# Optimization experiments

Hardware: AMD Instinct MI355X
Metric: run time of the kernel (lower is better)

## Reference

```python
import jax, jax.numpy as jnp
import numpy as np

THRESH = 0.5   # spike_args['thresh']
LENS = 0.5     # spike_args['lens'] (surrogate gradient window)
DECAY = 0.2    # spike_args['decay']
XISHUSPIKE = 0.5
XISHUADA = 0.2

@jax.custom_vjp
def spike_fn(v):
    return (v > THRESH).astype(v.dtype)

def _spike_fwd(v):
    return spike_fn(v), v

def _spike_bwd(v, g):
    # rectangular surrogate: pass grad where |v - thresh| < lens
    return (g * (jnp.abs(v - THRESH) < LENS).astype(g.dtype),)

spike_fn.defvjp(_spike_fwd, _spike_bwd)

def setup_inputs() -> dict:
    key = jax.random.key(0)
    k1, k2, k3, k4 = jax.random.split(key, 4)
    B, IN, OUT = 512, 2048, 2048
    x = jax.random.normal(k1, (B, IN), jnp.float32)
    W_fc = jax.random.normal(k2, (OUT, IN), jnp.float32) / np.sqrt(IN).astype(np.float32)
    b_fc = jnp.zeros((OUT,), jnp.float32)
    W_rec = jax.random.normal(k3, (OUT, OUT), jnp.float32) / np.sqrt(OUT).astype(np.float32)
    b_rec = jnp.zeros((OUT,), jnp.float32)
    eye = jnp.eye(OUT, dtype=jnp.int32)
    keep = jax.random.bernoulli(k4, 0.5, (OUT, OUT)).astype(jnp.int32)
    rec_mask = (1 - eye) * keep
    return {"x": x, "W_fc": W_fc, "b_fc": b_fc, "W_rec": W_rec,
            "b_rec": b_rec, "rec_mask": rec_mask, "spike_window": 16}

def reference(x, W_fc, b_fc, W_rec, b_rec, rec_mask, spike_window):
    # feed-forward drive is constant across the time loop (same x each step, noise off)
    ff = x @ W_fc.T + b_fc                      # [B, OUT]
    Wr = W_rec * rec_mask.astype(W_rec.dtype)    # masked recurrent weight (idempotent)
    z = jnp.zeros_like(ff)

    def step(carry, _):
        mem, spk, ath, ssum = carry
        ath = 0.9 * ath + XISHUSPIKE * spk
        mem_ff = mem * DECAY * (1.0 - spk) + ff - ath * XISHUADA
        s_ff = spike_fn(mem_ff)
        mem_r = spk @ Wr.T + b_rec
        s_r = spike_fn(mem_r)
        mem = mem_ff + mem_r
        spk = s_ff + s_r
        ssum = ssum + spk
        return (mem, spk, ath, ssum), None

    (mem, spk, ath, ssum), _ = jax.lax.scan(step, (z, z, z, z), None, length=spike_window)
    return ssum
```

## Files before the change

### kernel.cpp

```cpp
#include <hip/hip_runtime.h>


#pragma clang fp contract(off)

#define B_ROWS 512
#define N_OUT 2048
#define K_IN 2048
#define NSTEP 16
#define NPANEL 4
#define PANK 512
#define BK 16
#define TM 64
#define TN 128
#define ASTR 68
#define BSTR 132
#define NTILES (PANK / BK)

__global__ __launch_bounds__(256) void transpose_tile(
    const float* __restrict__ W, const int* __restrict__ mask,
    float* __restrict__ WT, int useMask)
{
    __shared__ float t[32][33];
    int kb = blockIdx.x * 32, nb = blockIdx.y * 32;
    int tx = threadIdx.x, ty = threadIdx.y;
#pragma unroll
    for (int r = 0; r < 32; r += 8) {
        size_t src = (size_t)(nb + ty + r) * K_IN + (kb + tx);
        float v = W[src];
        if (useMask) v *= (float)mask[src];
        t[ty + r][tx] = v;
    }
    __syncthreads();
#pragma unroll
    for (int r = 0; r < 32; r += 8)
        WT[(size_t)(kb + ty + r) * N_OUT + (nb + tx)] = t[tx][ty + r];
}

__global__ __launch_bounds__(256) void init_state(float* mem, float* ath,
                                                  float* ssum, float* spk) {
    int idx = blockIdx.x * 256 + threadIdx.x;
    mem[idx] = 0.0f; ath[idx] = 0.0f; ssum[idx] = 0.0f; spk[idx] = 0.0f;
}

__global__ __launch_bounds__(128) void gemm_panel(
    const float* __restrict__ A,
    const float* __restrict__ BT,
    float* __restrict__ Cp)
{
    __shared__ float As[2][BK][ASTR];
    __shared__ float Bs[2][BK][BSTR];
    const int tid = threadIdx.x;
    const int tx = tid & 15;
    const int ty = tid >> 4;
    const int n0 = blockIdx.x * TN;
    const int m0 = blockIdx.y * TM;
    const int pan = blockIdx.z;
    const int kbase = pan * PANK;

    const int sa_m = tid >> 1;
    const int sa_k = (tid & 1) * 8;
    const int sb_k = tid >> 3;
    const int sb_n = (tid & 7) * 16;

    float acc[8][8];
#pragma unroll
    for (int i = 0; i < 8; i++)
#pragma unroll
        for (int j = 0; j < 8; j++) acc[i][j] = 0.0f;

    const float* Abase = A + (size_t)(m0 + sa_m) * K_IN + kbase + sa_k;
    const float* Bbase = BT + (size_t)(kbase + sb_k) * N_OUT + n0 + sb_n;

    float4 ra0, ra1, rb0, rb1, rb2, rb3;
    ra0 = *(const float4*)(Abase);
    ra1 = *(const float4*)(Abase + 4);
    rb0 = *(const float4*)(Bbase);
    rb1 = *(const float4*)(Bbase + 4);
    rb2 = *(const float4*)(Bbase + 8);
    rb3 = *(const float4*)(Bbase + 12);
    {
        float av[8] = {ra0.x, ra0.y, ra0.z, ra0.w, ra1.x, ra1.y, ra1.z, ra1.w};
#pragma unroll
        for (int j = 0; j < 8; j++) As[0][sa_k + j][sa_m] = av[j];
        *(float4*)&Bs[0][sb_k][sb_n]      = rb0;
        *(float4*)&Bs[0][sb_k][sb_n + 4]  = rb1;
        *(float4*)&Bs[0][sb_k][sb_n + 8]  = rb2;
        *(float4*)&Bs[0][sb_k][sb_n + 12] = rb3;
    }
    __syncthreads();

    int buf = 0;
    for (int kt = 0; kt < NTILES; kt++) {
        if (kt + 1 < NTILES) {
            const float* Ab = Abase + (kt + 1) * BK;
            const float* Bb = Bbase + (size_t)(kt + 1) * BK * N_OUT;
            ra0 = *(const float4*)(Ab);
            ra1 = *(const float4*)(Ab + 4);
            rb0 = *(const float4*)(Bb);
            rb1 = *(const float4*)(Bb + 4);
            rb2 = *(const float4*)(Bb + 8);
            rb3 = *(const float4*)(Bb + 12);
        }
#pragma unroll
        for (int kk = 0; kk < BK; kk++) {
            float4 a0 = *(const float4*)&As[buf][kk][ty * 8];
            float4 a1 = *(const float4*)&As[buf][kk][ty * 8 + 4];
            float4 b0 = *(const float4*)&Bs[buf][kk][tx * 8];
            float4 b1 = *(const float4*)&Bs[buf][kk][tx * 8 + 4];
            float aa[8] = {a0.x, a0.y, a0.z, a0.w, a1.x, a1.y, a1.z, a1.w};
            float bb[8] = {b0.x, b0.y, b0.z, b0.w, b1.x, b1.y, b1.z, b1.w};
#pragma unroll
            for (int i = 0; i < 8; i++)
#pragma unroll
                for (int j = 0; j < 8; j++)
                    acc[i][j] = fmaf(aa[i], bb[j], acc[i][j]);
        }
        if (kt + 1 < NTILES) {
            __syncthreads();
            float av[8] = {ra0.x, ra0.y, ra0.z, ra0.w, ra1.x, ra1.y, ra1.z, ra1.w};
#pragma unroll
            for (int j = 0; j < 8; j++) As[buf ^ 1][sa_k + j][sa_m] = av[j];
            *(float4*)&Bs[buf ^ 1][sb_k][sb_n]      = rb0;
            *(float4*)&Bs[buf ^ 1][sb_k][sb_n + 4]  = rb1;
            *(float4*)&Bs[buf ^ 1][sb_k][sb_n + 8]  = rb2;
            *(float4*)&Bs[buf ^ 1][sb_k][sb_n + 12] = rb3;
            __syncthreads();
            buf ^= 1;
        }
    }

#pragma unroll
    for (int i = 0; i < 8; i++) {
        int row = m0 + ty * 8 + i;
        size_t off = (size_t)pan * (B_ROWS * N_OUT) + (size_t)row * N_OUT + n0 + tx * 8;
        *(float4*)(Cp + off)     = make_float4(acc[i][0], acc[i][1], acc[i][2], acc[i][3]);
        *(float4*)(Cp + off + 4) = make_float4(acc[i][4], acc[i][5], acc[i][6], acc[i][7]);
    }
}

__global__ __launch_bounds__(256) void ff_fold(
    const float* __restrict__ Cp, const float* __restrict__ b_fc,
    float* __restrict__ ff)
{
    const size_t P = (size_t)B_ROWS * N_OUT;
    size_t base = ((size_t)blockIdx.x * 256 + threadIdx.x) * 4;
    int n = (int)(base & (N_OUT - 1));
    float4 p0 = *(const float4*)(Cp + base);
    float4 p1 = *(const float4*)(Cp + P + base);
    float4 p2 = *(const float4*)(Cp + 2 * P + base);
    float4 p3 = *(const float4*)(Cp + 3 * P + base);
    float4 bv = *(const float4*)(b_fc + n);
    float4 o;
    o.x = ((p0.x + p1.x) + p2.x) + p3.x + 0.0f;
    o.x = (((p0.x + p1.x) + p2.x) + p3.x) + bv.x;
    o.y = (((p0.y + p1.y) + p2.y) + p3.y) + bv.y;
    o.z = (((p0.z + p1.z) + p2.z) + p3.z) + bv.z;
    o.w = (((p0.w + p1.w) + p2.w) + p3.w) + bv.w;
    *(float4*)(ff + base) = o;
}

__global__ __launch_bounds__(256) void fold_update(
    const float* __restrict__ Cp, const float* __restrict__ b_rec,
    const float* __restrict__ spk_in, const float* __restrict__ ff,
    float* __restrict__ mem, float* __restrict__ ath,
    float* __restrict__ ssum, float* __restrict__ spk_out,
    float* __restrict__ out, int last)
{
    const size_t P = (size_t)B_ROWS * N_OUT;
    size_t base = ((size_t)blockIdx.x * 256 + threadIdx.x) * 4;
    int n = (int)(base & (N_OUT - 1));
    float4 p0 = *(const float4*)(Cp + base);
    float4 p1 = *(const float4*)(Cp + P + base);
    float4 p2 = *(const float4*)(Cp + 2 * P + base);
    float4 p3 = *(const float4*)(Cp + 3 * P + base);
    float4 bv = *(const float4*)(b_rec + n);
    float4 sv = *(const float4*)(spk_in + base);
    float4 av = *(const float4*)(ath + base);
    float4 mv = *(const float4*)(mem + base);
    float4 fv = *(const float4*)(ff + base);
    float4 uv = *(const float4*)(ssum + base);

    float cr[4] = {(((p0.x + p1.x) + p2.x) + p3.x),
                   (((p0.y + p1.y) + p2.y) + p3.y),
                   (((p0.z + p1.z) + p2.z) + p3.z),
                   (((p0.w + p1.w) + p2.w) + p3.w)};
    float ba[4] = {bv.x, bv.y, bv.z, bv.w};
    float sa[4] = {sv.x, sv.y, sv.z, sv.w};
    float aa[4] = {av.x, av.y, av.z, av.w};
    float ma[4] = {mv.x, mv.y, mv.z, mv.w};
    float fa[4] = {fv.x, fv.y, fv.z, fv.w};
    float ua[4] = {uv.x, uv.y, uv.z, uv.w};
    float mo[4], ao[4], uo[4], so[4];
#pragma unroll
    for (int j = 0; j < 4; j++) {
        float memr  = cr[j] + ba[j];
        float sp    = sa[j];
        float t1    = aa[j] * 0.9f;
        float t2    = 0.5f * sp;
        float athn  = t1 + t2;
        float u1    = ma[j] * 0.2f;
        float u2    = 1.0f - sp;
        float u3    = u1 * u2;
        float u4    = u3 + fa[j];
        float u5    = athn * 0.2f;
        float memff = u4 - u5;
        float s_ff  = (memff > 0.5f) ? 1.0f : 0.0f;
        float s_r   = (memr  > 0.5f) ? 1.0f : 0.0f;
        mo[j] = memff + memr;
        ao[j] = athn;
        so[j] = s_ff + s_r;
        uo[j] = ua[j] + so[j];
    }
    *(float4*)(mem + base)     = make_float4(mo[0], mo[1], mo[2], mo[3]);
    *(float4*)(ath + base)     = make_float4(ao[0], ao[1], ao[2], ao[3]);
    *(float4*)(ssum + base)    = make_float4(uo[0], uo[1], uo[2], uo[3]);
    *(float4*)(spk_out + base) = make_float4(so[0], so[1], so[2], so[3]);
    if (last)
        *(float4*)(out + base) = make_float4(uo[0], uo[1], uo[2], uo[3]);
}

extern "C" void kernel_launch(void* const* d_in, const int* in_sizes, int n_in,
                              void* d_out, int out_size, void* d_ws, size_t ws_size,
                              hipStream_t stream) {
    const float* x      = (const float*)d_in[0];
    const float* W_fc   = (const float*)d_in[1];
    const float* b_fc   = (const float*)d_in[2];
    const float* W_rec  = (const float*)d_in[3];
    const float* b_rec  = (const float*)d_in[4];
    const int*   rmask  = (const int*)d_in[5];

    char* ws = (char*)d_ws;
    float* WT   = (float*)(ws);
    float* ff   = (float*)(ws + (16u << 20));
    float* mem  = (float*)(ws + (20u << 20));
    float* ath  = (float*)(ws + (24u << 20));
    float* ssum = (float*)(ws + (28u << 20));
    float* spkA = (float*)(ws + (32u << 20));
    float* spkB = (float*)(ws + (36u << 20));
    float* Cp   = (float*)(ws + (40u << 20));

    dim3 gridT(K_IN / 32, N_OUT / 32);
    dim3 blkT(32, 8);
    dim3 gridS((B_ROWS * N_OUT) / 256);
    dim3 gridG(N_OUT / TN, B_ROWS / TM, NPANEL);
    dim3 gridF((B_ROWS * N_OUT) / (256 * 4));

    transpose_tile<<<gridT, blkT, 0, stream>>>(W_fc, rmask, WT, 0);
    init_state<<<gridS, 256, 0, stream>>>(mem, ath, ssum, spkA);
    gemm_panel<<<gridG, 128, 0, stream>>>(x, WT, Cp);
    ff_fold<<<gridF, 256, 0, stream>>>(Cp, b_fc, ff);
    transpose_tile<<<gridT, blkT, 0, stream>>>(W_rec, rmask, WT, 1);

    for (int t = 0; t < NSTEP; t++) {
        const float* si = (t & 1) ? spkB : spkA;
        float*       so = (t & 1) ? spkA : spkB;
        gemm_panel<<<gridG, 128, 0, stream>>>(si, WT, Cp);
        fold_update<<<gridF, 256, 0, stream>>>(
            Cp, b_rec, si, ff, mem, ath, ssum, so, (float*)d_out, t == NSTEP - 1);
    }
}
```

Baseline: 1.390 ms.

## Restructure panel GEMM to single-wave blocks with direct global-to-LDS B loads

Rewrites the split-K panel GEMM as 64-thread single-wavefront blocks computing a 16x128 tile. Each lane owns two output columns. B tiles are streamed into LDS with global_load_lds and double buffered, with waitcnt used instead of __syncthreads. A rows are read straight from global memory as wave-uniform loads, replacing the shared-memory A tile. This is meant to raise occupancy and block count and to drop barrier and LDS-store overhead. In exchange, per-thread register reuse is much lower (2 columns per lane versus 8x8 before), so there are many more global reads of A and LDS reads per FMA.

```diff
diff --git a/kernel.cpp b/kernel.cpp
--- a/kernel.cpp
+++ b/kernel.cpp
@@ -10,11 +10,12 @@
 #define NPANEL 4
 #define PANK 512
 #define BK 16
-#define TM 64
+#define TM 16
 #define TN 128
-#define ASTR 68
-#define BSTR 132
 #define NTILES (PANK / BK)
+
+typedef const __attribute__((address_space(1))) void* gptr_t;
+typedef __attribute__((address_space(3))) void* lptr_t;
 
 __global__ __launch_bounds__(256) void transpose_tile(
     const float* __restrict__ W, const int* __restrict__ mask,
@@ -42,99 +43,85 @@
     mem[idx] = 0.0f; ath[idx] = 0.0f; ssum[idx] = 0.0f; spk[idx] = 0.0f;
 }
 
-__global__ __launch_bounds__(128) void gemm_panel(
+__global__ __launch_bounds__(64, 2) void gemm_panel(
     const float* __restrict__ A,
     const float* __restrict__ BT,
     float* __restrict__ Cp)
 {
-    __shared__ float As[2][BK][ASTR];
-    __shared__ float Bs[2][BK][BSTR];
-    const int tid = threadIdx.x;
-    const int tx = tid & 15;
-    const int ty = tid >> 4;
+    __shared__ float Bs[2][BK][TN];
+    const int lane = threadIdx.x;
     const int n0 = blockIdx.x * TN;
     const int m0 = blockIdx.y * TM;
     const int pan = blockIdx.z;
     const int kbase = pan * PANK;
 
-    const int sa_m = tid >> 1;
-    const int sa_k = (tid & 1) * 8;
-    const int sb_k = tid >> 3;
-    const int sb_n = (tid & 7) * 16;
-
-    float acc[8][8];
+    float acc[TM][2];
+#pragma unroll
+    for (int i = 0; i < TM; i++) { acc[i][0] = 0.0f; acc[i][1] = 0.0f; }
+
+    const float* src0 = BT + (size_t)(kbase + (lane >> 5)) * N_OUT
+                           + n0 + (lane & 31) * 4;
+
 #pragma unroll
     for (int i = 0; i < 8; i++)
-#pragma unroll
-        for (int j = 0; j < 8; j++) acc[i][j] = 0.0f;
-
-    const float* Abase = A + (size_t)(m0 + sa_m) * K_IN + kbase + sa_k;
-    const float* Bbase = BT + (size_t)(kbase + sb_k) * N_OUT + n0 + sb_n;
-
-    float4 ra0, ra1, rb0, rb1, rb2, rb3;
-    ra0 = *(const float4*)(Abase);
-    ra1 = *(const float4*)(Abase + 4);
-    rb0 = *(const float4*)(Bbase);
-    rb1 = *(const float4*)(Bbase + 4);
-    rb2 = *(const float4*)(Bbase + 8);
-    rb3 = *(const float4*)(Bbase + 12);
-    {
-        float av[8] = {ra0.x, ra0.y, ra0.z, ra0.w, ra1.x, ra1.y, ra1.z, ra1.w};
-#pragma unroll
-        for (int j = 0; j < 8; j++) As[0][sa_k + j][sa_m] = av[j];
-        *(float4*)&Bs[0][sb_k][sb_n]      = rb0;
-        *(float4*)&Bs[0][sb_k][sb_n + 4]  = rb1;
-        *(float4*)&Bs[0][sb_k][sb_n + 8]  = rb2;
-        *(float4*)&Bs[0][sb_k][sb_n + 12] = rb3;
-    }
-    __syncthreads();
+        __builtin_amdgcn_global_load_lds(
+            (gptr_t)(uintptr_t)(src0 + (size_t)(i * 2) * N_OUT),
+            (lptr_t)(uintptr_t)&Bs[0][i * 2][0], 16, 0, 0);
 
     int buf = 0;
     for (int kt = 0; kt < NTILES; kt++) {
         if (kt + 1 < NTILES) {
-            const float* Ab = Abase + (kt + 1) * BK;
-            const float* Bb = Bbase + (size_t)(kt + 1) * BK * N_OUT;
-            ra0 = *(const float4*)(Ab);
-            ra1 = *(const float4*)(Ab + 4);
-            rb0 = *(const float4*)(Bb);
-            rb1 = *(const float4*)(Bb + 4);
-            rb2 = *(const float4*)(Bb + 8);
-            rb3 = *(const float4*)(Bb + 12);
+#pragma unroll
+            for (int i = 0; i < 8; i++)
+                __builtin_amdgcn_global_load_lds(
+                    (gptr_t)(uintptr_t)(src0 + (size_t)((kt + 1) * BK + i * 2) * N_OUT),
+                    (lptr_t)(uintptr_t)&Bs[buf ^ 1][i * 2][0], 16, 0, 0);
+            asm volatile("s_waitcnt vmcnt(8)" ::: "memory");
+            __builtin_amdgcn_sched_barrier(0);
+        } else {
+            asm volatile("s_waitcnt vmcnt(0)" ::: "memory");
+            __builtin_amdgcn_sched_barrier(0);
         }
-#pragma unroll
-        for (int kk = 0; kk < BK; kk++) {
-            float4 a0 = *(const float4*)&As[buf][kk][ty * 8];
-            float4 a1 = *(const float4*)&As[buf][kk][ty * 8 + 4];
-            float4 b0 = *(const float4*)&Bs[buf][kk][tx * 8];
-            float4 b1 = *(const float4*)&Bs[buf][kk][tx * 8 + 4];
-            float aa[8] = {a0.x, a0.y, a0.z, a0.w, a1.x, a1.y, a1.z, a1.w};
-            float bb[8] = {b0.x, b0.y, b0.z, b0.w, b1.x, b1.y, b1.z, b1.w};
-#pragma unroll
-            for (int i = 0; i < 8; i++)
-#pragma unroll
-                for (int j = 0; j < 8; j++)
-                    acc[i][j] = fmaf(aa[i], bb[j], acc[i][j]);
+
+        float2 bv[BK];
+#pragma unroll
+        for (int kk = 0; kk < BK; kk++)
+            bv[kk] = *(const float2*)&Bs[buf][kk][lane * 2];
+
+        const float* Akt = A + (size_t)m0 * K_IN + kbase + kt * BK;
+#pragma unroll
+        for (int mg = 0; mg < 4; mg++) {
+            float av[4][BK];
+#pragma unroll
+            for (int r = 0; r < 4; r++) {
+                const float* Ar = Akt + (size_t)(mg * 4 + r) * K_IN;
+                float4 q0 = *(const float4*)(Ar + 0);
+                float4 q1 = *(const float4*)(Ar + 4);
+                float4 q2 = *(const float4*)(Ar + 8);
+                float4 q3 = *(const float4*)(Ar + 12);
+                av[r][0]  = q0.x; av[r][1]  = q0.y; av[r][2]  = q0.z; av[r][3]  = q0.w;
+                av[r][4]  = q1.x; av[r][5]  = q1.y; av[r][6]  = q1.z; av[r][7]  = q1.w;
+                av[r][8]  = q2.x; av[r][9]  = q2.y; av[r][10] = q2.z; av[r][11] = q2.w;
+                av[r][12] = q3.x; av[r][13] = q3.y; av[r][14] = q3.z; av[r][15] = q3.w;
+            }
+#pragma unroll
+            for (int kk = 0; kk < BK; kk++) {
+                float bx = bv[kk].x, by = bv[kk].y;
+#pragma unroll
+                for (int r = 0; r < 4; r++) {
+                    acc[mg * 4 + r][0] = fmaf(av[r][kk], bx, acc[mg * 4 + r][0]);
+                    acc[mg * 4 + r][1] = fmaf(av[r][kk], by, acc[mg * 4 + r][1]);
+                }
+            }
         }
-        if (kt + 1 < NTILES) {
-            __syncthreads();
-            float av[8] = {ra0.x, ra0.y, ra0.z, ra0.w, ra1.x, ra1.y, ra1.z, ra1.w};
-#pragma unroll
-            for (int j = 0; j < 8; j++) As[buf ^ 1][sa_k + j][sa_m] = av[j];
-            *(float4*)&Bs[buf ^ 1][sb_k][sb_n]      = rb0;
-            *(float4*)&Bs[buf ^ 1][sb_k][sb_n + 4]  = rb1;
-            *(float4*)&Bs[buf ^ 1][sb_k][sb_n + 8]  = rb2;
-            *(float4*)&Bs[buf ^ 1][sb_k][sb_n + 12] = rb3;
-            __syncthreads();
-            buf ^= 1;
-        }
-    }
-
-#pragma unroll
-    for (int i = 0; i < 8; i++) {
-        int row = m0 + ty * 8 + i;
-        size_t off = (size_t)pan * (B_ROWS * N_OUT) + (size_t)row * N_OUT + n0 + tx * 8;
-        *(float4*)(Cp + off)     = make_float4(acc[i][0], acc[i][1], acc[i][2], acc[i][3]);
-        *(float4*)(Cp + off + 4) = make_float4(acc[i][4], acc[i][5], acc[i][6], acc[i][7]);
+        buf ^= 1;
+    }
+
+    const size_t P = (size_t)B_ROWS * N_OUT;
+#pragma unroll
+    for (int i = 0; i < TM; i++) {
+        size_t off = (size_t)pan * P + (size_t)(m0 + i) * N_OUT + n0 + lane * 2;
+        *(float2*)(Cp + off) = make_float2(acc[i][0], acc[i][1]);
     }
 }
 
@@ -151,7 +138,6 @@
     float4 p3 = *(const float4*)(Cp + 3 * P + base);
     float4 bv = *(const float4*)(b_fc + n);
     float4 o;
-    o.x = ((p0.x + p1.x) + p2.x) + p3.x + 0.0f;
     o.x = (((p0.x + p1.x) + p2.x) + p3.x) + bv.x;
     o.y = (((p0.y + p1.y) + p2.y) + p3.y) + bv.y;
     o.z = (((p0.z + p1.z) + p2.z) + p3.z) + bv.z;
@@ -247,14 +233,14 @@
 
     transpose_tile<<<gridT, blkT, 0, stream>>>(W_fc, rmask, WT, 0);
     init_state<<<gridS, 256, 0, stream>>>(mem, ath, ssum, spkA);
-    gemm_panel<<<gridG, 128, 0, stream>>>(x, WT, Cp);
+    gemm_panel<<<gridG, 64, 0, stream>>>(x, WT, Cp);
     ff_fold<<<gridF, 256, 0, stream>>>(Cp, b_fc, ff);
     transpose_tile<<<gridT, blkT, 0, stream>>>(W_rec, rmask, WT, 1);
 
     for (int t = 0; t < NSTEP; t++) {
         const float* si = (t & 1) ? spkB : spkA;
         float*       so = (t & 1) ? spkA : spkB;
-        gemm_panel<<<gridG, 128, 0, stream>>>(si, WT, Cp);
+        gemm_panel<<<gridG, 64, 0, stream>>>(si, WT, Cp);
         fold_update<<<gridF, 256, 0, stream>>>(
             Cp, b_rec, si, ff, mem, ath, ssum, so, (float*)d_out, t == NSTEP - 1);
     }
```

New measurement: 1.693 ms. 1.22x slower.
